# Kernel optimization log

Hardware: AMD Instinct MI355X
Metric: run time of the kernel (lower is better)

The kernel has to match this reference:

```python
import jax, jax.numpy as jnp
import numpy as np

B, S, H, F, E, K = 2, 2048, 1024, 4096, 8, 2

def setup_inputs() -> dict:
    key = jax.random.key(0)
    ks = jax.random.split(key, 8)
    x = jax.random.normal(ks[0], (B, S, H), dtype=jnp.float32)
    # top_k list stacked on leading axis K; probs as from a softmax-topk router
    selected_probs = jax.random.uniform(ks[1], (K, B, S, 1), dtype=jnp.float32)
    selected_experts = jax.random.randint(ks[2], (K, B, S, 1), 0, E).astype(jnp.int32)
    scale = 0.02
    w1 = jax.random.normal(ks[3], (E, H, F), dtype=jnp.float32) * scale
    b1 = jnp.zeros((E, F), dtype=jnp.float32)
    w2 = jax.random.normal(ks[4], (E, F, H), dtype=jnp.float32) * scale
    b2 = jnp.zeros((E, H), dtype=jnp.float32)
    return {"input": x, "selected_probs": selected_probs,
            "selected_experts": selected_experts,
            "w1": w1, "b1": b1, "w2": w2, "b2": b2}

def reference(input, selected_probs, selected_experts, w1, b1, w2, b2):
    # Dense all-experts FFN: every expert processes every token.
    # h: [E, B, S, F]
    h = jax.nn.gelu(jnp.einsum('bsh,ehf->ebsf', input, w1) + b1[:, None, None, :])
    # expert_outputs: [E, B, S, H]
    expert_out = jnp.einsum('ebsf,efh->ebsh', h, w2) + b2[:, None, None, :]
    # combine weight per expert: sum_k probs_k * (sel_k == e)  -> [E, B, S, 1]
    eids = jnp.arange(E, dtype=selected_experts.dtype)
    mask = (selected_experts[:, None] == eids[None, :, None, None, None]).astype(input.dtype)  # [K,E,B,S,1]
    combine_w = (selected_probs[:, None] * mask).sum(axis=0)  # [E,B,S,1]
    return (combine_w * expert_out).sum(axis=0)  # [B,S,H]
```

## Files before the change

kernel.cpp:

```cpp
#include <hip/hip_runtime.h>
#include <hip/hip_bf16.h>
#include <stdint.h>

#define B_ 2
#define S_ 2048
#define H_ 1024
#define F_ 4096
#define E_ 8
#define KTOP_ 2
#define NTOK (B_*S_)
#define NPAIR (KTOP_*NTOK)
#define NPAIR_PAD (NPAIR+256)

static const size_t WS_XG   = 131072;
static const size_t SZ_XG   = (size_t)NPAIR_PAD * H_ * 2;
static const size_t WS_W1T  = WS_XG + SZ_XG;
static const size_t SZ_W1T  = (size_t)E_ * F_ * H_ * 2;
static const size_t WS_W2T  = WS_W1T + SZ_W1T;
static const size_t SZ_W2T  = (size_t)E_ * H_ * F_ * 2;
static const size_t WS_HBUF = WS_W2T + SZ_W2T;
static const size_t SZ_HBUF = (size_t)NPAIR_PAD * F_ * 2;
static const size_t WS_YBUF = WS_HBUF + SZ_HBUF;

typedef __attribute__((ext_vector_type(8))) short bf16x8;
typedef __attribute__((ext_vector_type(4))) float f32x4;

__device__ __forceinline__ unsigned short f2bf(float f) {
  unsigned int u = __float_as_uint(f);
  u += 0x7fffu + ((u >> 16) & 1u);
  return (unsigned short)(u >> 16);
}

__device__ __forceinline__ void load_lds16(const void* g, void* l) {
  __builtin_amdgcn_global_load_lds(
      (const __attribute__((address_space(1))) unsigned int*)g,
      (__attribute__((address_space(3))) unsigned int*)l, 16, 0, 0);
}

__global__ void k_init(int* meta) {
  if (threadIdx.x < 32) meta[threadIdx.x] = 0;
}

__global__ void k_count(const int* __restrict__ sel, int* meta) {
  int i = blockIdx.x * 256 + threadIdx.x;
  if (i < NPAIR) atomicAdd(&meta[sel[i]], 1);
}

__global__ void k_scan(int* meta) {
  if (threadIdx.x == 0) {
    int acc = 0, t256 = 0, t128 = 0;
    for (int e = 0; e < E_; e++) {
      meta[16 + e] = acc;
      int c = meta[e];
      for (int r0 = 0; r0 < c; r0 += 256) meta[32 + (t256++)] = (e << 13) | r0;
      for (int r0 = 0; r0 < c; r0 += 128) meta[72 + (t128++)] = (e << 13) | r0;
      acc += c;
    }
    meta[24] = acc;
    meta[25] = t256;
    meta[26] = t128;
  }
}

__global__ void k_fill(const int* __restrict__ sel, const float* __restrict__ probs,
                       int* meta, int* __restrict__ tok, int* __restrict__ slot,
                       float* __restrict__ prob) {
  int i = blockIdx.x * 256 + threadIdx.x;
  if (i < NPAIR) {
    int e = sel[i];
    int pos = meta[16 + e] + atomicAdd(&meta[8 + e], 1);
    tok[pos]  = i & (NTOK - 1);
    slot[pos] = i;
    prob[pos] = probs[i];
  }
}

__global__ void k_gather(const float* __restrict__ x, const int* __restrict__ tok,
                         unsigned short* __restrict__ Xg) {
  int p = blockIdx.x, t = threadIdx.x;
  int token = tok[p];
  float4 v = ((const float4*)(x + (size_t)token * H_))[t];
  ushort4 o;
  o.x = f2bf(v.x); o.y = f2bf(v.y); o.z = f2bf(v.z); o.w = f2bf(v.w);
  ((ushort4*)(Xg + (size_t)p * H_))[t] = o;
}

__global__ void k_transpose(const float* __restrict__ src, unsigned short* __restrict__ dst,
                            int R, int C) {
  __shared__ float tile[64][65];
  int e = blockIdx.z;
  size_t c0 = (size_t)blockIdx.x * 64, r0 = (size_t)blockIdx.y * 64;
  int t = threadIdx.x;
  int r = t >> 2, q = t & 3;
  const float4* s = (const float4*)(src + ((size_t)e * R + r0 + r) * C + c0 + q * 16);
  float4 v0 = s[0], v1 = s[1], v2 = s[2], v3 = s[3];
  float* tp = &tile[r][q * 16];
  tp[0]=v0.x; tp[1]=v0.y; tp[2]=v0.z; tp[3]=v0.w;
  tp[4]=v1.x; tp[5]=v1.y; tp[6]=v1.z; tp[7]=v1.w;
  tp[8]=v2.x; tp[9]=v2.y; tp[10]=v2.z; tp[11]=v2.w;
  tp[12]=v3.x; tp[13]=v3.y; tp[14]=v3.z; tp[15]=v3.w;
  __syncthreads();
  unsigned short* d = dst + ((size_t)e * C + c0) * R + r0;
#pragma unroll
  for (int i = 0; i < 8; i++) {
    int chunk = t + 256 * i;
    int c = chunk >> 5, j = chunk & 31;
    ushort2 o;
    o.x = f2bf(tile[2 * j][c]);
    o.y = f2bf(tile[2 * j + 1][c]);
    *(ushort2*)(d + (size_t)c * R + 2 * j) = o;
  }
}


template <int K, int MREP, int NREP, int DBASE, int NIDX, int EP>
__global__ __launch_bounds__(512, EP == 0 ? 2 : 4) void k_gemm2p(
    const short* __restrict__ Aall, const short* __restrict__ Wt,
    const float* __restrict__ bias, const int* __restrict__ meta,
    unsigned short* __restrict__ Hbuf, float* __restrict__ ybuf,
    const int* __restrict__ slotA, const float* __restrict__ prob) {
  constexpr int BM = 2 * MREP * 16;
  constexpr int BN = 4 * NREP * 16;
  constexpr int NT = K / 64;
  constexpr int ABYTES = BM * 128;
  constexpr int BBYTES = BN * 128;
  constexpr int BUF = ABYTES + BBYTES;
  constexpr int LOADS = BUF / (512 * 16);
  constexpr int ALOADS = ABYTES / (512 * 16);
  constexpr int NFULL = (EP == 0) ? F_ : H_;

  __shared__ __align__(1024) char lds[2 * BUF];

  int tile = blockIdx.y;
  if (tile >= meta[NIDX]) return;
  int d  = meta[DBASE + tile];
  int e  = d >> 13, r0 = d & 8191;
  int ne = meta[e];
  int p0 = meta[16 + e] + r0;
  int n0 = blockIdx.x * BN;
  const char* A0 = (const char*)(Aall + (size_t)p0 * K);
  const char* B0 = (const char*)(Wt + ((size_t)e * NFULL + n0) * K);

  int t = threadIdx.x, lane = t & 63, wid = t >> 6;
  int wr = wid >> 2, wc = wid & 3, g = lane >> 4, l15 = lane & 15;
  f32x4 acc[MREP][NREP] = {};

  auto stage = [&](int kt, char* dst) {
    const char* sa = A0 + kt * 128;
    const char* sb = B0 + kt * 128;
#pragma unroll
    for (int l = 0; l < LOADS; l++) {
      int off = l * 8192 + t * 16;
      if (l < ALOADS) {
        int row = off >> 7, inb = off & 127;
        load_lds16(sa + (size_t)row * (K * 2) + (inb ^ ((row & 7) << 4)), dst + off);
      } else {
        int o2 = off - ABYTES;
        int row = o2 >> 7, inb = o2 & 127;
        load_lds16(sb + (size_t)row * (K * 2) + (inb ^ ((row & 7) << 4)), dst + off);
      }
    }
  };

  stage(0, lds);
  __syncthreads();
  int cur = 0;
  for (int kt = 0; kt < NT; kt++) {
    const char* ab = lds + cur * BUF;
    const char* bb = ab + ABYTES;
    if (kt + 1 < NT) stage(kt + 1, lds + (cur ^ 1) * BUF);
    __builtin_amdgcn_s_setprio(1);
#pragma unroll
    for (int kk = 0; kk < 2; kk++) {
      bf16x8 af[MREP], bf[NREP];
#pragma unroll
      for (int m = 0; m < MREP; m++) {
        int row = wr * (MREP * 16) + m * 16 + l15;
        af[m] = *(const bf16x8*)(ab + row * 128 + ((kk * 64 + g * 16) ^ ((row & 7) << 4)));
      }
#pragma unroll
      for (int n = 0; n < NREP; n++) {
        int row = wc * (NREP * 16) + n * 16 + l15;
        bf[n] = *(const bf16x8*)(bb + row * 128 + ((kk * 64 + g * 16) ^ ((row & 7) << 4)));
      }
#pragma unroll
      for (int m = 0; m < MREP; m++)
#pragma unroll
        for (int n = 0; n < NREP; n++)
          acc[m][n] = __builtin_amdgcn_mfma_f32_16x16x32_bf16(af[m], bf[n], acc[m][n], 0, 0, 0);
    }
    __builtin_amdgcn_s_setprio(0);
    __syncthreads();
    cur ^= 1;
  }

  if (EP == 0) {
#pragma unroll
    for (int n = 0; n < NREP; n++) {
      int col = n0 + wc * (NREP * 16) + n * 16 + l15;
      float bv = bias[e * F_ + col];
#pragma unroll
      for (int m = 0; m < MREP; m++) {
        int rbase = wr * (MREP * 16) + m * 16 + g * 4;
#pragma unroll
        for (int r = 0; r < 4; r++) {
          int row = rbase + r;
          if (r0 + row < ne) {
            float x = acc[m][n][r] + bv;
            float x2 = x * x;
            float ttt = x * (2.302118f + 0.1029518f * x2);
            ttt = fminf(ttt, 60.f);
            float u = __builtin_amdgcn_exp2f(ttt);
            float rr = __frcp_rn(1.f + u);
            Hbuf[(size_t)(p0 + row) * F_ + col] = f2bf(x * u * rr);
          }
        }
      }
    }
  } else {
#pragma unroll
    for (int n = 0; n < NREP; n++) {
      int col = n0 + wc * (NREP * 16) + n * 16 + l15;
      float bv = bias[e * H_ + col];
#pragma unroll
      for (int m = 0; m < MREP; m++) {
        int rbase = wr * (MREP * 16) + m * 16 + g * 4;
#pragma unroll
        for (int r = 0; r < 4; r++) {
          int row = rbase + r;
          if (r0 + row < ne) {
            int p = p0 + row;
            ybuf[(size_t)slotA[p] * H_ + col] = (acc[m][n][r] + bv) * prob[p];
          }
        }
      }
    }
  }
}

__global__ void k_combine(const float* __restrict__ yb, float* __restrict__ out) {
  size_t i = (size_t)blockIdx.x * 256 + threadIdx.x;
  float4 a = ((const float4*)yb)[i];
  float4 b = ((const float4*)(yb + (size_t)NTOK * H_))[i];
  float4 o;
  o.x = a.x + b.x; o.y = a.y + b.y; o.z = a.z + b.z; o.w = a.w + b.w;
  ((float4*)out)[i] = o;
}

extern "C" void kernel_launch(void* const* d_in, const int* in_sizes, int n_in,
                              void* d_out, int out_size, void* d_ws, size_t ws_size,
                              hipStream_t stream) {
  const float* x     = (const float*)d_in[0];
  const float* probs = (const float*)d_in[1];
  const int*   sel   = (const int*)d_in[2];
  const float* w1    = (const float*)d_in[3];
  const float* b1    = (const float*)d_in[4];
  const float* w2    = (const float*)d_in[5];
  const float* b2    = (const float*)d_in[6];
  float* out = (float*)d_out;

  char* W = (char*)d_ws;
  int*   meta = (int*)W;
  int*   tok  = (int*)(W + 4096);
  int*   slot = (int*)(W + 36864);
  float* prob = (float*)(W + 69632);
  unsigned short* Xg  = (unsigned short*)(W + WS_XG);
  short* w1t = (short*)(W + WS_W1T);
  short* w2t = (short*)(W + WS_W2T);
  unsigned short* Hb  = (unsigned short*)(W + WS_HBUF);
  float* yb  = (float*)(W + WS_YBUF);

  k_init<<<1, 256, 0, stream>>>(meta);
  k_count<<<NPAIR / 256, 256, 0, stream>>>(sel, meta);
  k_scan<<<1, 64, 0, stream>>>(meta);
  k_fill<<<NPAIR / 256, 256, 0, stream>>>(sel, probs, meta, tok, slot, prob);
  k_gather<<<NPAIR, 256, 0, stream>>>(x, tok, Xg);
  k_transpose<<<dim3(F_ / 64, H_ / 64, E_), 256, 0, stream>>>(w1, (unsigned short*)w1t, H_, F_);
  k_transpose<<<dim3(H_ / 64, F_ / 64, E_), 256, 0, stream>>>(w2, (unsigned short*)w2t, F_, H_);
  k_gemm2p<H_, 8, 4, 32, 25, 0><<<dim3(F_ / 256, 40), 512, 0, stream>>>(
      (const short*)Xg, w1t, b1, meta, Hb, yb, slot, prob);
  k_gemm2p<F_, 4, 2, 72, 26, 1><<<dim3(H_ / 128, 72), 512, 0, stream>>>(
      (const short*)Hb, w2t, b2, meta, Hb, yb, slot, prob);
  k_combine<<<(NTOK * H_ / 4) / 256, 256, 0, stream>>>(yb, out);
}
```

Measured before the change: 478.2 us.

## Replace first expert GEMM with hand-scheduled 8-phase pipelined kernel

Replaces the first grouped GEMM (X·W1 + GELU) with a dedicated kernel that splits each 256x256 tile's k-step into four quadrant MFMA phases. LDS fragment reads and global-to-LDS prefetches are interleaved between them using explicit barriers and vmcnt/lgkmcnt waits, with a 128 KB double buffer for A and B. The goal is to hide global load and LDS read latency behind matrix math instead of relying on the single-barrier double-buffer loop. In exchange it adds many barriers and hand-tuned wait counts, which are fragile, and the large LDS footprint limits occupancy. The second GEMM is only specialised, with its GELU branch removed.

```diff
diff --git a/kernel.cpp b/kernel.cpp
--- a/kernel.cpp
+++ b/kernel.cpp
@@ -112,13 +112,146 @@
   }
 }
 
-
-template <int K, int MREP, int NREP, int DBASE, int NIDX, int EP>
-__global__ __launch_bounds__(512, EP == 0 ? 2 : 4) void k_gemm2p(
+__device__ __forceinline__ float gelu_f(float x) {
+  float x2 = x * x;
+  float ttt = x * (2.302118f + 0.1029518f * x2);
+  ttt = fminf(ttt, 60.f);
+  float u = __builtin_amdgcn_exp2f(ttt);
+  float rr = __frcp_rn(1.f + u);
+  return x * u * rr;
+}
+
+template <int K>
+__global__ __launch_bounds__(512, 2) void k_gemm8p(
     const short* __restrict__ Aall, const short* __restrict__ Wt,
     const float* __restrict__ bias, const int* __restrict__ meta,
-    unsigned short* __restrict__ Hbuf, float* __restrict__ ybuf,
-    const int* __restrict__ slotA, const float* __restrict__ prob) {
+    unsigned short* __restrict__ Hbuf) {
+  constexpr int NI = K / 128;
+  __shared__ __align__(1024) char lds[131072];
+  int tile = blockIdx.y;
+  if (tile >= meta[25]) return;
+  int dsc = meta[32 + tile];
+  int e = dsc >> 13, r0 = dsc & 8191;
+  int ne = meta[e];
+  int p0 = meta[16 + e] + r0;
+  int n0 = blockIdx.x * 256;
+  const char* A0 = (const char*)(Aall + (size_t)p0 * K);
+  const char* B0 = (const char*)(Wt + ((size_t)e * F_ + n0) * K);
+  int t = threadIdx.x, lane = t & 63, wid = t >> 6;
+  int wr = wid >> 2, wc = wid & 3, g = lane >> 4, l15 = lane & 15;
+  f32x4 acc[8][4] = {};
+
+  auto stage = [&](int mat, int db, int kt) {
+    const char* src = mat ? B0 : A0;
+    char* dst = lds + db * 65536 + mat * 32768;
+#pragma unroll
+    for (int l = 0; l < 4; l++) {
+      int off = l * 8192 + t * 16;
+      int row = off >> 7, inb = off & 127;
+      load_lds16(src + (size_t)row * (K * 2) + kt * 128 + (inb ^ ((row & 7) << 4)), dst + off);
+    }
+  };
+  bf16x8 af[2][4], af2[2][4], bfv[2][2], bf2[2][2];
+  auto readA = [&](int db, int mh, bf16x8 (&dv)[2][4]) {
+#pragma unroll
+    for (int kk = 0; kk < 2; kk++)
+#pragma unroll
+      for (int m = 0; m < 4; m++) {
+        int row = wr * 128 + mh * 64 + m * 16 + l15;
+        dv[kk][m] = *(const bf16x8*)(lds + db * 65536 + row * 128 +
+                                     ((kk * 64 + g * 16) ^ ((row & 7) << 4)));
+      }
+  };
+  auto readB = [&](int db, int nh, bf16x8 (&dv)[2][2]) {
+#pragma unroll
+    for (int kk = 0; kk < 2; kk++)
+#pragma unroll
+      for (int n = 0; n < 2; n++) {
+        int row = wc * 64 + (nh * 2 + n) * 16 + l15;
+        dv[kk][n] = *(const bf16x8*)(lds + db * 65536 + 32768 + row * 128 +
+                                     ((kk * 64 + g * 16) ^ ((row & 7) << 4)));
+      }
+  };
+  auto quad = [&](int mh, int nh, bf16x8 (&Av)[2][4], bf16x8 (&Bv)[2][2]) {
+    __builtin_amdgcn_s_setprio(1);
+#pragma unroll
+    for (int kk = 0; kk < 2; kk++)
+#pragma unroll
+      for (int m = 0; m < 4; m++)
+#pragma unroll
+        for (int n = 0; n < 2; n++)
+          acc[mh * 4 + m][nh * 2 + n] = __builtin_amdgcn_mfma_f32_16x16x32_bf16(
+              Av[kk][m], Bv[kk][n], acc[mh * 4 + m][nh * 2 + n], 0, 0, 0);
+    __builtin_amdgcn_s_setprio(0);
+  };
+  auto bar = []() { __builtin_amdgcn_s_barrier(); };
+  auto lg0 = []() { asm volatile("s_waitcnt lgkmcnt(0)" ::: "memory"); };
+  auto vm8 = []() { asm volatile("s_waitcnt vmcnt(8)" ::: "memory"); };
+  auto vm0 = []() { asm volatile("s_waitcnt vmcnt(0)" ::: "memory"); };
+
+  stage(1, 0, 0); stage(0, 0, 0); stage(1, 1, 1); stage(0, 1, 1);
+  vm8(); bar();
+
+  for (int i = 0; i < NI - 1; i++) {
+    int kn0 = 2 * i + 2, kn1 = 2 * i + 3;
+    readA(0, 0, af); readB(0, 0, bfv);
+    bar(); lg0(); quad(0, 0, af, bfv); bar();
+    readB(0, 1, bf2);
+    bar(); lg0(); quad(0, 1, af, bf2); bar();
+    readA(0, 1, af2); stage(1, 0, kn0);
+    bar(); lg0(); quad(1, 0, af2, bfv); bar();
+    stage(0, 0, kn0); vm8();
+    bar(); quad(1, 1, af2, bf2); bar();
+    readA(1, 0, af); readB(1, 0, bfv);
+    bar(); lg0(); quad(0, 0, af, bfv); bar();
+    readB(1, 1, bf2);
+    bar(); lg0(); quad(0, 1, af, bf2); bar();
+    readA(1, 1, af2); stage(1, 1, kn1);
+    bar(); lg0(); quad(1, 0, af2, bfv); bar();
+    stage(0, 1, kn1); vm8();
+    bar(); quad(1, 1, af2, bf2); bar();
+  }
+  readA(0, 0, af); readB(0, 0, bfv);
+  bar(); lg0(); quad(0, 0, af, bfv); bar();
+  readB(0, 1, bf2);
+  bar(); lg0(); quad(0, 1, af, bf2); bar();
+  readA(0, 1, af2);
+  bar(); lg0(); quad(1, 0, af2, bfv); bar();
+  vm0();
+  bar(); quad(1, 1, af2, bf2); bar();
+  readA(1, 0, af); readB(1, 0, bfv);
+  bar(); lg0(); quad(0, 0, af, bfv); bar();
+  readB(1, 1, bf2);
+  bar(); lg0(); quad(0, 1, af, bf2); bar();
+  readA(1, 1, af2);
+  bar(); lg0(); quad(1, 0, af2, bfv); bar();
+  quad(1, 1, af2, bf2);
+
+#pragma unroll
+  for (int n = 0; n < 4; n++) {
+    int col = n0 + wc * 64 + n * 16 + l15;
+    float bv = bias[e * F_ + col];
+#pragma unroll
+    for (int m = 0; m < 8; m++) {
+      int rbase = wr * 128 + m * 16 + g * 4;
+#pragma unroll
+      for (int r = 0; r < 4; r++) {
+        int row = rbase + r;
+        if (r0 + row < ne) {
+          float x = acc[m][n][r] + bv;
+          Hbuf[(size_t)(p0 + row) * F_ + col] = f2bf(gelu_f(x));
+        }
+      }
+    }
+  }
+}
+
+template <int K, int MREP, int NREP, int DBASE, int NIDX>
+__global__ __launch_bounds__(512, 4) void k_gemm2p(
+    const short* __restrict__ Aall, const short* __restrict__ Wt,
+    const float* __restrict__ bias, const int* __restrict__ meta,
+    float* __restrict__ ybuf, const int* __restrict__ slotA,
+    const float* __restrict__ prob) {
   constexpr int BM = 2 * MREP * 16;
   constexpr int BN = 4 * NREP * 16;
   constexpr int NT = K / 64;
@@ -127,19 +260,18 @@
   constexpr int BUF = ABYTES + BBYTES;
   constexpr int LOADS = BUF / (512 * 16);
   constexpr int ALOADS = ABYTES / (512 * 16);
-  constexpr int NFULL = (EP == 0) ? F_ : H_;
 
   __shared__ __align__(1024) char lds[2 * BUF];
 
   int tile = blockIdx.y;
   if (tile >= meta[NIDX]) return;
-  int d  = meta[DBASE + tile];
-  int e  = d >> 13, r0 = d & 8191;
+  int d = meta[DBASE + tile];
+  int e = d >> 13, r0 = d & 8191;
   int ne = meta[e];
   int p0 = meta[16 + e] + r0;
   int n0 = blockIdx.x * BN;
   const char* A0 = (const char*)(Aall + (size_t)p0 * K);
-  const char* B0 = (const char*)(Wt + ((size_t)e * NFULL + n0) * K);
+  const char* B0 = (const char*)(Wt + ((size_t)e * H_ + n0) * K);
 
   int t = threadIdx.x, lane = t & 63, wid = t >> 6;
   int wr = wid >> 2, wc = wid & 3, g = lane >> 4, l15 = lane & 15;
@@ -172,66 +304,41 @@
     __builtin_amdgcn_s_setprio(1);
 #pragma unroll
     for (int kk = 0; kk < 2; kk++) {
-      bf16x8 af[MREP], bf[NREP];
+      bf16x8 afv[MREP], bfv[NREP];
 #pragma unroll
       for (int m = 0; m < MREP; m++) {
         int row = wr * (MREP * 16) + m * 16 + l15;
-        af[m] = *(const bf16x8*)(ab + row * 128 + ((kk * 64 + g * 16) ^ ((row & 7) << 4)));
+        afv[m] = *(const bf16x8*)(ab + row * 128 + ((kk * 64 + g * 16) ^ ((row & 7) << 4)));
       }
 #pragma unroll
       for (int n = 0; n < NREP; n++) {
         int row = wc * (NREP * 16) + n * 16 + l15;
-        bf[n] = *(const bf16x8*)(bb + row * 128 + ((kk * 64 + g * 16) ^ ((row & 7) << 4)));
+        bfv[n] = *(const bf16x8*)(bb + row * 128 + ((kk * 64 + g * 16) ^ ((row & 7) << 4)));
       }
 #pragma unroll
       for (int m = 0; m < MREP; m++)
 #pragma unroll
         for (int n = 0; n < NREP; n++)
-          acc[m][n] = __builtin_amdgcn_mfma_f32_16x16x32_bf16(af[m], bf[n], acc[m][n], 0, 0, 0);
+          acc[m][n] = __builtin_amdgcn_mfma_f32_16x16x32_bf16(afv[m], bfv[n], acc[m][n], 0, 0, 0);
     }
     __builtin_amdgcn_s_setprio(0);
     __syncthreads();
     cur ^= 1;
   }
 
-  if (EP == 0) {
-#pragma unroll
-    for (int n = 0; n < NREP; n++) {
-      int col = n0 + wc * (NREP * 16) + n * 16 + l15;
-      float bv = bias[e * F_ + col];
-#pragma unroll
-      for (int m = 0; m < MREP; m++) {
-        int rbase = wr * (MREP * 16) + m * 16 + g * 4;
-#pragma unroll
-        for (int r = 0; r < 4; r++) {
-          int row = rbase + r;
-          if (r0 + row < ne) {
-            float x = acc[m][n][r] + bv;
-            float x2 = x * x;
-            float ttt = x * (2.302118f + 0.1029518f * x2);
-            ttt = fminf(ttt, 60.f);
-            float u = __builtin_amdgcn_exp2f(ttt);
-            float rr = __frcp_rn(1.f + u);
-            Hbuf[(size_t)(p0 + row) * F_ + col] = f2bf(x * u * rr);
-          }
-        }
-      }
-    }
-  } else {
-#pragma unroll
-    for (int n = 0; n < NREP; n++) {
-      int col = n0 + wc * (NREP * 16) + n * 16 + l15;
-      float bv = bias[e * H_ + col];
-#pragma unroll
-      for (int m = 0; m < MREP; m++) {
-        int rbase = wr * (MREP * 16) + m * 16 + g * 4;
-#pragma unroll
-        for (int r = 0; r < 4; r++) {
-          int row = rbase + r;
-          if (r0 + row < ne) {
-            int p = p0 + row;
-            ybuf[(size_t)slotA[p] * H_ + col] = (acc[m][n][r] + bv) * prob[p];
-          }
+#pragma unroll
+  for (int n = 0; n < NREP; n++) {
+    int col = n0 + wc * (NREP * 16) + n * 16 + l15;
+    float bv = bias[e * H_ + col];
+#pragma unroll
+    for (int m = 0; m < MREP; m++) {
+      int rbase = wr * (MREP * 16) + m * 16 + g * 4;
+#pragma unroll
+      for (int r = 0; r < 4; r++) {
+        int row = rbase + r;
+        if (r0 + row < ne) {
+          int p = p0 + row;
+          ybuf[(size_t)slotA[p] * H_ + col] = (acc[m][n][r] + bv) * prob[p];
         }
       }
     }
@@ -277,9 +384,9 @@
   k_gather<<<NPAIR, 256, 0, stream>>>(x, tok, Xg);
   k_transpose<<<dim3(F_ / 64, H_ / 64, E_), 256, 0, stream>>>(w1, (unsigned short*)w1t, H_, F_);
   k_transpose<<<dim3(H_ / 64, F_ / 64, E_), 256, 0, stream>>>(w2, (unsigned short*)w2t, F_, H_);
-  k_gemm2p<H_, 8, 4, 32, 25, 0><<<dim3(F_ / 256, 40), 512, 0, stream>>>(
-      (const short*)Xg, w1t, b1, meta, Hb, yb, slot, prob);
-  k_gemm2p<F_, 4, 2, 72, 26, 1><<<dim3(H_ / 128, 72), 512, 0, stream>>>(
-      (const short*)Hb, w2t, b2, meta, Hb, yb, slot, prob);
+  k_gemm8p<H_><<<dim3(F_ / 256, 40), 512, 0, stream>>>(
+      (const short*)Xg, w1t, b1, meta, Hb);
+  k_gemm2p<F_, 4, 2, 72, 26><<<dim3(H_ / 128, 72), 512, 0, stream>>>(
+      (const short*)Hb, w2t, b2, meta, yb, slot, prob);
   k_combine<<<(NTOK * H_ / 4) / 256, 256, 0, stream>>>(yb, out);
 }
```

New measurement: 469.4 us. About the same (-1.8%).

## Unify both expert GEMMs into one 128x128 tile kernel with K-step 32

Applied to the files above, without the earlier changes.

Replaces the templated 512-thread GEMM with a single 256-thread kernel using 128x128 output tiles, 4x4 MFMA fragments per wave, and a 32-element K step with a 64-byte-row XOR-swizzled LDS layout. The first GEMM now uses 128-row expert tiles instead of 256-row tiles, so the 256-row scan descriptors are dropped. The aim is better occupancy and less padding waste for small expert groups. The cost is smaller per-iteration loads with more barriers, and less weight reuse per tile in GEMM1.

```diff
diff --git a/kernel.cpp b/kernel.cpp
--- a/kernel.cpp
+++ b/kernel.cpp
@@ -48,16 +48,14 @@
 
 __global__ void k_scan(int* meta) {
   if (threadIdx.x == 0) {
-    int acc = 0, t256 = 0, t128 = 0;
+    int acc = 0, t128 = 0;
     for (int e = 0; e < E_; e++) {
       meta[16 + e] = acc;
       int c = meta[e];
-      for (int r0 = 0; r0 < c; r0 += 256) meta[32 + (t256++)] = (e << 13) | r0;
       for (int r0 = 0; r0 < c; r0 += 128) meta[72 + (t128++)] = (e << 13) | r0;
       acc += c;
     }
     meta[24] = acc;
-    meta[25] = t256;
     meta[26] = t128;
   }
 }
@@ -112,119 +110,114 @@
   }
 }
 
-
-template <int K, int MREP, int NREP, int DBASE, int NIDX, int EP>
-__global__ __launch_bounds__(512, EP == 0 ? 2 : 4) void k_gemm2p(
+__device__ __forceinline__ float gelu_f(float x) {
+  float x2 = x * x;
+  float ttt = x * (2.302118f + 0.1029518f * x2);
+  ttt = fminf(ttt, 60.f);
+  float u = __builtin_amdgcn_exp2f(ttt);
+  float rr = __frcp_rn(1.f + u);
+  return x * u * rr;
+}
+
+template <int K, int EP>
+__global__ __launch_bounds__(256, 4) void k_gemmdb(
     const short* __restrict__ Aall, const short* __restrict__ Wt,
     const float* __restrict__ bias, const int* __restrict__ meta,
     unsigned short* __restrict__ Hbuf, float* __restrict__ ybuf,
     const int* __restrict__ slotA, const float* __restrict__ prob) {
-  constexpr int BM = 2 * MREP * 16;
-  constexpr int BN = 4 * NREP * 16;
-  constexpr int NT = K / 64;
-  constexpr int ABYTES = BM * 128;
-  constexpr int BBYTES = BN * 128;
-  constexpr int BUF = ABYTES + BBYTES;
-  constexpr int LOADS = BUF / (512 * 16);
-  constexpr int ALOADS = ABYTES / (512 * 16);
+  constexpr int NT = K / 32;
   constexpr int NFULL = (EP == 0) ? F_ : H_;
-
-  __shared__ __align__(1024) char lds[2 * BUF];
+  __shared__ __align__(1024) char lds[2][16384];
 
   int tile = blockIdx.y;
-  if (tile >= meta[NIDX]) return;
-  int d  = meta[DBASE + tile];
-  int e  = d >> 13, r0 = d & 8191;
+  if (tile >= meta[26]) return;
+  int dsc = meta[72 + tile];
+  int e = dsc >> 13, r0 = dsc & 8191;
   int ne = meta[e];
   int p0 = meta[16 + e] + r0;
-  int n0 = blockIdx.x * BN;
+  int n0 = blockIdx.x * 128;
   const char* A0 = (const char*)(Aall + (size_t)p0 * K);
   const char* B0 = (const char*)(Wt + ((size_t)e * NFULL + n0) * K);
 
   int t = threadIdx.x, lane = t & 63, wid = t >> 6;
-  int wr = wid >> 2, wc = wid & 3, g = lane >> 4, l15 = lane & 15;
-  f32x4 acc[MREP][NREP] = {};
+  int wr = wid >> 1, wc = wid & 1, g = lane >> 4, l15 = lane & 15;
+  f32x4 acc[4][4] = {};
 
   auto stage = [&](int kt, char* dst) {
-    const char* sa = A0 + kt * 128;
-    const char* sb = B0 + kt * 128;
-#pragma unroll
-    for (int l = 0; l < LOADS; l++) {
-      int off = l * 8192 + t * 16;
-      if (l < ALOADS) {
-        int row = off >> 7, inb = off & 127;
-        load_lds16(sa + (size_t)row * (K * 2) + (inb ^ ((row & 7) << 4)), dst + off);
-      } else {
-        int o2 = off - ABYTES;
-        int row = o2 >> 7, inb = o2 & 127;
-        load_lds16(sb + (size_t)row * (K * 2) + (inb ^ ((row & 7) << 4)), dst + off);
-      }
+#pragma unroll
+    for (int l = 0; l < 2; l++) {
+      int off = l * 4096 + t * 16;
+      int o2 = off ^ (((off >> 7) & 7) << 4);
+      int row = o2 >> 6, cb = o2 & 63;
+      load_lds16(A0 + (size_t)row * (K * 2) + kt * 64 + cb, dst + off);
+    }
+#pragma unroll
+    for (int l = 0; l < 2; l++) {
+      int off = l * 4096 + t * 16;
+      int o2 = off ^ (((off >> 7) & 7) << 4);
+      int row = o2 >> 6, cb = o2 & 63;
+      load_lds16(B0 + (size_t)row * (K * 2) + kt * 64 + cb, dst + 8192 + off);
     }
   };
 
-  stage(0, lds);
+  auto compute = [&](const char* ab) {
+    const char* bb = ab + 8192;
+    bf16x8 af[4], bf[4];
+#pragma unroll
+    for (int m = 0; m < 4; m++) {
+      int a = (wr * 64 + m * 16 + l15) * 64 + g * 16;
+      af[m] = *(const bf16x8*)(ab + (a ^ (((a >> 7) & 7) << 4)));
+    }
+#pragma unroll
+    for (int n = 0; n < 4; n++) {
+      int b = (wc * 64 + n * 16 + l15) * 64 + g * 16;
+      bf[n] = *(const bf16x8*)(bb + (b ^ (((b >> 7) & 7) << 4)));
+    }
+    __builtin_amdgcn_s_setprio(1);
+#pragma unroll
+    for (int m = 0; m < 4; m++)
+#pragma unroll
+      for (int n = 0; n < 4; n++)
+        acc[m][n] = __builtin_amdgcn_mfma_f32_16x16x32_bf16(af[m], bf[n], acc[m][n], 0, 0, 0);
+    __builtin_amdgcn_s_setprio(0);
+  };
+
+  stage(0, lds[0]);
   __syncthreads();
   int cur = 0;
   for (int kt = 0; kt < NT; kt++) {
-    const char* ab = lds + cur * BUF;
-    const char* bb = ab + ABYTES;
-    if (kt + 1 < NT) stage(kt + 1, lds + (cur ^ 1) * BUF);
-    __builtin_amdgcn_s_setprio(1);
-#pragma unroll
-    for (int kk = 0; kk < 2; kk++) {
-      bf16x8 af[MREP], bf[NREP];
-#pragma unroll
-      for (int m = 0; m < MREP; m++) {
-        int row = wr * (MREP * 16) + m * 16 + l15;
-        af[m] = *(const bf16x8*)(ab + row * 128 + ((kk * 64 + g * 16) ^ ((row & 7) << 4)));
-      }
-#pragma unroll
-      for (int n = 0; n < NREP; n++) {
-        int row = wc * (NREP * 16) + n * 16 + l15;
-        bf[n] = *(const bf16x8*)(bb + row * 128 + ((kk * 64 + g * 16) ^ ((row & 7) << 4)));
-      }
-#pragma unroll
-      for (int m = 0; m < MREP; m++)
-#pragma unroll
-        for (int n = 0; n < NREP; n++)
-          acc[m][n] = __builtin_amdgcn_mfma_f32_16x16x32_bf16(af[m], bf[n], acc[m][n], 0, 0, 0);
-    }
-    __builtin_amdgcn_s_setprio(0);
+    if (kt + 1 < NT) stage(kt + 1, lds[cur ^ 1]);
+    compute(lds[cur]);
     __syncthreads();
     cur ^= 1;
   }
 
   if (EP == 0) {
 #pragma unroll
-    for (int n = 0; n < NREP; n++) {
-      int col = n0 + wc * (NREP * 16) + n * 16 + l15;
+    for (int n = 0; n < 4; n++) {
+      int col = n0 + wc * 64 + n * 16 + l15;
       float bv = bias[e * F_ + col];
 #pragma unroll
-      for (int m = 0; m < MREP; m++) {
-        int rbase = wr * (MREP * 16) + m * 16 + g * 4;
+      for (int m = 0; m < 4; m++) {
+        int rbase = wr * 64 + m * 16 + g * 4;
 #pragma unroll
         for (int r = 0; r < 4; r++) {
           int row = rbase + r;
           if (r0 + row < ne) {
             float x = acc[m][n][r] + bv;
-            float x2 = x * x;
-            float ttt = x * (2.302118f + 0.1029518f * x2);
-            ttt = fminf(ttt, 60.f);
-            float u = __builtin_amdgcn_exp2f(ttt);
-            float rr = __frcp_rn(1.f + u);
-            Hbuf[(size_t)(p0 + row) * F_ + col] = f2bf(x * u * rr);
+            Hbuf[(size_t)(p0 + row) * F_ + col] = f2bf(gelu_f(x));
           }
         }
       }
     }
   } else {
 #pragma unroll
-    for (int n = 0; n < NREP; n++) {
-      int col = n0 + wc * (NREP * 16) + n * 16 + l15;
+    for (int n = 0; n < 4; n++) {
+      int col = n0 + wc * 64 + n * 16 + l15;
       float bv = bias[e * H_ + col];
 #pragma unroll
-      for (int m = 0; m < MREP; m++) {
-        int rbase = wr * (MREP * 16) + m * 16 + g * 4;
+      for (int m = 0; m < 4; m++) {
+        int rbase = wr * 64 + m * 16 + g * 4;
 #pragma unroll
         for (int r = 0; r < 4; r++) {
           int row = rbase + r;
@@ -277,9 +270,9 @@
   k_gather<<<NPAIR, 256, 0, stream>>>(x, tok, Xg);
   k_transpose<<<dim3(F_ / 64, H_ / 64, E_), 256, 0, stream>>>(w1, (unsigned short*)w1t, H_, F_);
   k_transpose<<<dim3(H_ / 64, F_ / 64, E_), 256, 0, stream>>>(w2, (unsigned short*)w2t, F_, H_);
-  k_gemm2p<H_, 8, 4, 32, 25, 0><<<dim3(F_ / 256, 40), 512, 0, stream>>>(
+  k_gemmdb<H_, 0><<<dim3(F_ / 128, 72), 256, 0, stream>>>(
       (const short*)Xg, w1t, b1, meta, Hb, yb, slot, prob);
-  k_gemm2p<F_, 4, 2, 72, 26, 1><<<dim3(H_ / 128, 72), 512, 0, stream>>>(
+  k_gemmdb<F_, 1><<<dim3(H_ / 128, 72), 256, 0, stream>>>(
       (const short*)Hb, w2t, b2, meta, Hb, yb, slot, prob);
   k_combine<<<(NTOK * H_ / 4) / 256, 256, 0, stream>>>(yb, out);
 }
```

Result: faster. 454.6 us (-4.9%).
